# Kernel tuning notes

Measured on AMD Instinct MI355X. Metric: run time of the kernel, lower is better.

The kernel has to match this reference:

```python
import jax, jax.numpy as jnp
import numpy as np
from jax.scipy.special import digamma

# Dims (see init_kwargs): pose P=4 -> D=16, stem A=128, primary caps B=32,
# classes C=10, class-caps kernel K=6 (== primary feature map size), 3 routing iters.
P, D, A, B, C, K, ITER = 4, 16, 128, 32, 10, 6, 3
N = B * K * K                                    # input capsules routed to each class capsule
ALPHA0, KAPPA0, NU0 = 1.0, 1.0, float(D + 1)     # Dirichlet/Normal-Wishart priors (m0=0, Psi0=I, cov='diag')
BN_EPS, EPS = 1e-5, 1e-8


def conv2d(x, w, s):
    return jax.lax.conv_general_dilated(x, w, (s, s), 'VALID',
                                        dimension_numbers=('NCHW', 'OIHW', 'NCHW'))


def bn(x, gamma, beta, axes):
    # batch-norm with batch statistics (training-mode math)
    mu = x.mean(axes, keepdims=True)
    var = x.var(axes, keepdims=True)
    return (x - mu) * jax.lax.rsqrt(var + BN_EPS) * gamma + beta


def setup_inputs():
    key = jax.random.key(0)
    ks = jax.random.split(key, 4)
    f32 = jnp.float32
    x = jax.random.normal(ks[0], (128, 3, 32, 32), dtype=f32)
    conv1_w = jax.random.normal(ks[1], (A, 3, 5, 5), dtype=f32) * 0.1
    bn1_g = jnp.ones((A,), f32); bn1_b = jnp.zeros((A,), f32)
    prim_w = jax.random.normal(ks[2], (B * D + B, A, 3, 3), dtype=f32) * 0.05
    bna_g = jnp.ones((B,), f32); bna_b = jnp.zeros((B,), f32)
    bnp_g = jnp.ones((B,), f32); bnp_b = jnp.zeros((B,), f32)
    W_ij = jax.random.normal(ks[3], (B, C, K, K, P, P), dtype=f32) * 0.3
    return dict(x=x, conv1_w=conv1_w, bn1_g=bn1_g, bn1_b=bn1_b, prim_w=prim_w,
                bna_g=bna_g, bna_b=bna_b, bnp_g=bnp_g, bnp_b=bnp_b, W_ij=W_ij)


def _vb_stats(Ra, V):
    # Ra: (b,N,C) responsibility * input activation; V: (b,N,C,D) votes
    Nj = Ra.sum(1) + EPS                                         # (b,C)
    xbar = jnp.einsum('bnc,bncd->bcd', Ra, V) / Nj[..., None]    # weighted vote mean
    diff = V - xbar[:, None]
    sigma = jnp.einsum('bnc,bncd->bcd', Ra, diff * diff) / Nj[..., None]  # diag cov
    kappa = KAPPA0 + Nj
    m = Nj[..., None] * xbar / kappa[..., None]                  # posterior mean (m0 = 0)
    nu = NU0 + Nj
    Psi = 1.0 + Nj[..., None] * sigma + (KAPPA0 * Nj / kappa)[..., None] * xbar * xbar  # Psi0 = I (diag)
    return Nj, kappa, m, nu, Psi


def _expectations(Nj, nu, Psi, d_idx):
    alpha = ALPHA0 + Nj
    E_lnpi = digamma(alpha) - digamma(alpha.sum(-1, keepdims=True))
    E_lnLam = (digamma(0.5 * (nu[..., None] + 1.0 - d_idx)).sum(-1)
               + D * jnp.log(2.0) - jnp.log(Psi).sum(-1))
    return E_lnpi, E_lnLam


def reference(x, conv1_w, bn1_g, bn1_b, prim_w, bna_g, bna_b, bnp_g, bnp_b, W_ij):
    b = x.shape[0]
    # --- stem: Conv5x5/s2 + BN + ReLU ---
    h = conv2d(x, conv1_w, 2)                                    # (b,A,14,14)
    h = jax.nn.relu(bn(h, bn1_g[None, :, None, None], bn1_b[None, :, None, None], (0, 2, 3)))
    # --- primary capsules: Conv3x3/s2 -> poses + activations ---
    pc = conv2d(h, prim_w, 2)                                    # (b,B*D+B,6,6)
    poses, a = pc[:, :B * D], pc[:, B * D:]
    a = jax.nn.sigmoid(bn(a, bna_g[None, :, None, None], bna_b[None, :, None, None], (0, 2, 3)))
    poses = bn(poses.reshape(b, B, D, K, K),
               bnp_g[None, :, None, None, None], bnp_b[None, :, None, None, None], (0, 2, 3, 4))
    poses = poses.reshape(b, B, P, P, K, K)
    # --- class capsules: votes V = W_ij @ pose, kernel covers whole 6x6 map ---
    V = jnp.einsum('icxypq,biqrxy->bicxypr', W_ij, poses)        # (b,B,C,K,K,P,P)
    V = V.transpose(0, 1, 3, 4, 2, 5, 6).reshape(b, N, C, D)
    a_i = a.reshape(b, N)
    # --- variational Bayes routing (diag Normal-Wishart, ITER iterations) ---
    d_idx = jnp.arange(1, D + 1, dtype=x.dtype)
    R = jnp.full((b, N, C), 1.0 / C, dtype=x.dtype)
    for t in range(ITER):
        Nj, kappa, m, nu, Psi = _vb_stats(R * a_i[:, :, None], V)
        if t < ITER - 1:
            E_lnpi, E_lnLam = _expectations(Nj, nu, Psi, d_idx)
            dm = V - m[:, None]
            quad = D / kappa[:, None, :] + nu[:, None, :] * jnp.einsum('bncd,bcd->bnc', dm * dm, 1.0 / Psi)
            lnp = (E_lnpi[:, None] + 0.5 * E_lnLam[:, None]
                   - 0.5 * D * jnp.log(2.0 * jnp.pi) - 0.5 * quad)
            R = jax.nn.softmax(lnp, axis=-1)
    E_lnpi, E_lnLam = _expectations(Nj, nu, Psi, d_idx)
    logits = E_lnpi + 0.5 * E_lnLam                              # (b,C)
    yhat = jax.nn.sigmoid(bn(logits, 1.0, 0.0, (0,)))            # BatchNorm1d(affine=False)
    return yhat
```

## Files before the change

### kernel.cpp

```cpp
#include <hip/hip_runtime.h>
#include <hip/hip_bf16.h>

#define NB 128
#define AA 128
#define BB 32
#define CC 10
#define KK 6
#define DD 16
#define NN 1152
#define H1 14
#define CH2 544
#define NG 4608
#define KG 1152
#define MG 576

typedef short bfrag8 __attribute__((ext_vector_type(8)));
typedef float facc4 __attribute__((ext_vector_type(4)));

__device__ __forceinline__ unsigned short f2bf(float f) {
    unsigned u = __float_as_uint(f);
    u += 0x7FFF + ((u >> 16) & 1);
    return (unsigned short)(u >> 16);
}
__device__ __forceinline__ float bf2f(unsigned short s) {
    return __uint_as_float(((unsigned)s) << 16);
}

__global__ __launch_bounds__(256, 3) void k_conv1(const float* __restrict__ x,
                                                  const float* __restrict__ w,
                                                  float* __restrict__ h,
                                                  float* __restrict__ part1s,
                                                  float* __restrict__ part1q) {
    __shared__ __align__(16) float sX[3][7][32];
    __shared__ float sWf[AA * 75];
    __shared__ float sS[128], sQ[128];
    const int p = blockIdx.x;
    const int b = blockIdx.y;
    const int tid = threadIdx.x;
    for (int j = tid; j < AA * 75; j += 256) sWf[j] = w[j];
    for (int j = tid; j < 3 * 7 * 32; j += 256) {
        int col = j & 31; int t2 = j >> 5; int row = t2 % 7; int ic = t2 / 7;
        sX[ic][row][col] = x[b * 3072 + ic * 1024 + (4 * p + row) * 32 + col];
    }
    __syncthreads();
    const int oc = tid & 127, ry = tid >> 7;
    const int r = 2 * p + ry;
    float acc[14];
#pragma unroll
    for (int j = 0; j < 14; ++j) acc[j] = 0.f;
    const float* wr = sWf + oc * 75;
#pragma unroll
    for (int ic = 0; ic < 3; ++ic) {
#pragma unroll
        for (int ky = 0; ky < 5; ++ky) {
            const float* xr = &sX[ic][2 * ry + ky][0];
            float row[32];
#pragma unroll
            for (int q = 0; q < 8; ++q) {
                float4 v = *reinterpret_cast<const float4*>(xr + q * 4);
                row[q * 4 + 0] = v.x; row[q * 4 + 1] = v.y;
                row[q * 4 + 2] = v.z; row[q * 4 + 3] = v.w;
            }
            float w0 = wr[ic * 25 + ky * 5 + 0];
            float w1 = wr[ic * 25 + ky * 5 + 1];
            float w2 = wr[ic * 25 + ky * 5 + 2];
            float w3 = wr[ic * 25 + ky * 5 + 3];
            float w4 = wr[ic * 25 + ky * 5 + 4];
#pragma unroll
            for (int ox = 0; ox < 14; ++ox) {
                float s = acc[ox];
                s = fmaf(row[2 * ox + 0], w0, s);
                s = fmaf(row[2 * ox + 1], w1, s);
                s = fmaf(row[2 * ox + 2], w2, s);
                s = fmaf(row[2 * ox + 3], w3, s);
                s = fmaf(row[2 * ox + 4], w4, s);
                acc[ox] = s;
            }
        }
    }
    float* out = h + ((size_t)(b * AA + oc) * 14 + r) * 14;
#pragma unroll
    for (int q = 0; q < 7; ++q)
        *reinterpret_cast<float2*>(out + q * 2) = make_float2(acc[q * 2], acc[q * 2 + 1]);
    float s_th = 0.f, q_th = 0.f;
#pragma unroll
    for (int ox = 0; ox < 14; ++ox) { s_th += acc[ox]; q_th = fmaf(acc[ox], acc[ox], q_th); }
    if (ry == 1) { sS[oc] = s_th; sQ[oc] = q_th; }
    __syncthreads();
    if (ry == 0) {
        int blk = p * 128 + b;
        part1s[oc * 896 + blk] = s_th + sS[oc];
        part1q[oc * 896 + blk] = q_th + sQ[oc];
    }
}

__device__ __forceinline__ void blk_reduce2(float& s, float& s2, int tid) {
#pragma unroll
    for (int o = 32; o > 0; o >>= 1) { s += __shfl_down(s, o); s2 += __shfl_down(s2, o); }
    __shared__ float ls[4], lq[4];
    int lane = tid & 63, wid = tid >> 6;
    if (lane == 0) { ls[wid] = s; lq[wid] = s2; }
    __syncthreads();
    if (tid == 0) {
        s = ls[0] + ls[1] + ls[2] + ls[3];
        s2 = lq[0] + lq[1] + lq[2] + lq[3];
    }
}

__global__ void k_bnred1(const float* __restrict__ part1s, const float* __restrict__ part1q,
                         const float* __restrict__ g, const float* __restrict__ be,
                         float* __restrict__ bn1) {
    int c = blockIdx.x;
    int tid = threadIdx.x;
    float s = 0.f, s2 = 0.f;
    for (int j = tid; j < 896; j += 256) { s += part1s[c * 896 + j]; s2 += part1q[c * 896 + j]; }
    blk_reduce2(s, s2, tid);
    if (tid == 0) {
        const float n = (float)(NB * 196);
        float mu = s / n;
        float var = s2 / n - mu * mu;
        float sc = g[c] * rsqrtf(var + 1e-5f);
        bn1[c] = sc;
        bn1[AA + c] = be[c] - mu * sc;
    }
}

__global__ void k_pim(const float* __restrict__ w, const float* __restrict__ h,
                      const float* __restrict__ bn1,
                      unsigned short* __restrict__ Ah, unsigned short* __restrict__ Al,
                      unsigned short* __restrict__ Bh, unsigned short* __restrict__ Bl) {
    const int blk = blockIdx.x;
    const int tid = threadIdx.x;
    if (blk < 324) {
        int t = blk * 256 + tid;
        int row = t / (KG / 8), seg = t % (KG / 8);
        alignas(16) unsigned short hi[8], lo[8];
        if (row < CH2) {
            const float* src = w + (size_t)row * KG + seg * 8;
#pragma unroll
            for (int j = 0; j < 8; ++j) {
                float v = src[j];
                unsigned short hh = f2bf(v);
                hi[j] = hh;
                lo[j] = f2bf(v - bf2f(hh));
            }
        } else {
#pragma unroll
            for (int j = 0; j < 8; ++j) { hi[j] = 0; lo[j] = 0; }
        }
        *reinterpret_cast<uint4*>(Ah + (size_t)row * KG + seg * 8) = *reinterpret_cast<const uint4*>(hi);
        *reinterpret_cast<uint4*>(Al + (size_t)row * KG + seg * 8) = *reinterpret_cast<const uint4*>(lo);
        return;
    }
    __shared__ float sBn1[2 * AA];
    sBn1[tid] = bn1[tid];
    __syncthreads();
    int t = (blk - 324) * 256 + tid;
    int n = t / (KG / 8), seg = t % (KG / 8);
    int b = n / 36, xy = n % 36;
    int oy = xy / 6, ox = xy % 6;
    const float* hb = h + (size_t)b * (AA * 196) + (2 * oy) * 14 + 2 * ox;
    alignas(16) unsigned short hi[8], lo[8];
#pragma unroll
    for (int j = 0; j < 8; ++j) {
        int k = seg * 8 + j;
        int ic = k / 9, kk = k - ic * 9;
        int ky = kk / 3, kx = kk - ky * 3;
        float v = hb[ic * 196 + ky * 14 + kx];
        v = fmaxf(fmaf(v, sBn1[ic], sBn1[AA + ic]), 0.f);
        unsigned short hh = f2bf(v);
        hi[j] = hh;
        lo[j] = f2bf(v - bf2f(hh));
    }
    *reinterpret_cast<uint4*>(Bh + (size_t)n * KG + seg * 8) = *reinterpret_cast<const uint4*>(hi);
    *reinterpret_cast<uint4*>(Bl + (size_t)n * KG + seg * 8) = *reinterpret_cast<const uint4*>(lo);
}

__global__ __launch_bounds__(256, 4) void k_gemm(const unsigned short* __restrict__ Ah,
                                                 const unsigned short* __restrict__ Al,
                                                 const unsigned short* __restrict__ Bh,
                                                 const unsigned short* __restrict__ Bl,
                                                 float* __restrict__ pcT,
                                                 float* __restrict__ part2) {
    __shared__ alignas(16) unsigned short sAh[64][44], sAl[64][44];
    __shared__ alignas(16) unsigned short sBh[64][44], sBl[64][44];
    __shared__ float sRed[128];
    const int s = blockIdx.x;
    const int k8 = s & 7, j = s >> 3;
    const int jm = j / 9;
    const int y = k8 + 8 * jm;
    const int xg = j - 9 * jm;
    const int oc0 = xg * 64;
    const int n0 = y * 64;
    const int tid = threadIdx.x;
    const int lane = tid & 63, wv = tid >> 6;
    const int wm = wv >> 1, wn = wv & 1;
    const int quad = lane >> 4, r16 = lane & 15;
    const int srow = tid >> 2, sseg = tid & 3;

    facc4 acc[2][2] = {};
    const size_t gA = (size_t)(oc0 + srow) * KG + sseg * 8;
    const size_t gB = (size_t)(n0 + srow) * KG + sseg * 8;

    uint4 vAh = *reinterpret_cast<const uint4*>(Ah + gA);
    uint4 vAl = *reinterpret_cast<const uint4*>(Al + gA);
    uint4 vBh = *reinterpret_cast<const uint4*>(Bh + gB);
    uint4 vBl = *reinterpret_cast<const uint4*>(Bl + gB);

    for (int ks = 0; ks < KG / 32; ++ks) {
        __syncthreads();
        *reinterpret_cast<uint4*>(&sAh[srow][sseg * 8]) = vAh;
        *reinterpret_cast<uint4*>(&sAl[srow][sseg * 8]) = vAl;
        *reinterpret_cast<uint4*>(&sBh[srow][sseg * 8]) = vBh;
        *reinterpret_cast<uint4*>(&sBl[srow][sseg * 8]) = vBl;
        __syncthreads();
        if (ks + 1 < KG / 32) {
            const int k0n = (ks + 1) * 32;
            vAh = *reinterpret_cast<const uint4*>(Ah + gA + k0n);
            vAl = *reinterpret_cast<const uint4*>(Al + gA + k0n);
            vBh = *reinterpret_cast<const uint4*>(Bh + gB + k0n);
            vBl = *reinterpret_cast<const uint4*>(Bl + gB + k0n);
        }
        bfrag8 ah[2], al[2], bh[2], bl[2];
#pragma unroll
        for (int i = 0; i < 2; ++i) {
            ah[i] = *reinterpret_cast<const bfrag8*>(&sAh[wm * 32 + i * 16 + r16][quad * 8]);
            al[i] = *reinterpret_cast<const bfrag8*>(&sAl[wm * 32 + i * 16 + r16][quad * 8]);
            bh[i] = *reinterpret_cast<const bfrag8*>(&sBh[wn * 32 + i * 16 + r16][quad * 8]);
            bl[i] = *reinterpret_cast<const bfrag8*>(&sBl[wn * 32 + i * 16 + r16][quad * 8]);
        }
#pragma unroll
        for (int i = 0; i < 2; ++i)
#pragma unroll
            for (int jj = 0; jj < 2; ++jj) {
                acc[i][jj] = __builtin_amdgcn_mfma_f32_16x16x32_bf16(ah[i], bh[jj], acc[i][jj], 0, 0, 0);
                acc[i][jj] = __builtin_amdgcn_mfma_f32_16x16x32_bf16(ah[i], bl[jj], acc[i][jj], 0, 0, 0);
                acc[i][jj] = __builtin_amdgcn_mfma_f32_16x16x32_bf16(al[i], bh[jj], acc[i][jj], 0, 0, 0);
            }
    }
#pragma unroll
    for (int i = 0; i < 2; ++i) {
        int oc_base = oc0 + wm * 32 + i * 16 + quad * 4;
        if (oc_base >= CH2) continue;
#pragma unroll
        for (int jj = 0; jj < 2; ++jj) {
            int n = n0 + wn * 32 + jj * 16 + r16;
            *reinterpret_cast<facc4*>(pcT + (size_t)n * CH2 + oc_base) = acc[i][jj];
        }
    }
    if (xg < 8) {
        float ps[2], pq[2];
#pragma unroll
        for (int i = 0; i < 2; ++i) {
            float sv = 0.f, qv = 0.f;
#pragma unroll
            for (int jj = 0; jj < 2; ++jj)
#pragma unroll
                for (int comp = 0; comp < 4; ++comp) {
                    float v = acc[i][jj][comp];
                    sv += v; qv = fmaf(v, v, qv);
                }
#pragma unroll
            for (int o = 32; o > 0; o >>= 1) { sv += __shfl_down(sv, o); qv += __shfl_down(qv, o); }
            ps[i] = sv; pq[i] = qv;
        }
        if (lane == 0) {
#pragma unroll
            for (int i = 0; i < 2; ++i) { sRed[wv * 4 + i * 2 + 0] = ps[i]; sRed[wv * 4 + i * 2 + 1] = pq[i]; }
        }
        __syncthreads();
        if (tid < 8) {
            int wm_ = tid >> 2, i_ = (tid >> 1) & 1, sel = tid & 1;
            float v = sRed[(2 * wm_) * 4 + i_ * 2 + sel] + sRed[(2 * wm_ + 1) * 4 + i_ * 2 + sel];
            int g = xg * 4 + wm_ * 2 + i_;
            part2[sel * 2304 + g * 72 + y] = v;
        }
    } else {
        if (wm == 0) {
#pragma unroll
            for (int i = 0; i < 2; ++i)
#pragma unroll
                for (int comp = 0; comp < 4; ++comp) {
                    float v0 = acc[i][0][comp], v1 = acc[i][1][comp];
                    float sv = v0 + v1;
                    float qv = fmaf(v0, v0, v1 * v1);
#pragma unroll
                    for (int o = 8; o > 0; o >>= 1) {
                        sv += __shfl_down(sv, o, 16);
                        qv += __shfl_down(qv, o, 16);
                    }
                    if (r16 == 0) {
                        int idx = ((wv * 4 + quad) * 2 + i) * 4 + comp;
                        sRed[idx] = sv;
                        sRed[64 + idx] = qv;
                    }
                }
        }
        __syncthreads();
        if (tid < 64) {
            int ch = tid >> 1, sel = tid & 1;
            int i_ = ch >> 4, rem = ch & 15, quad_ = rem >> 2, comp_ = rem & 3;
            int base = sel * 64;
            float v = sRed[base + ((0 * 4 + quad_) * 2 + i_) * 4 + comp_] +
                      sRed[base + ((1 * 4 + quad_) * 2 + i_) * 4 + comp_];
            part2[4608 + sel * 2304 + ch * 72 + y] = v;
        }
    }
}

__device__ __forceinline__ float digammaf_(float x) {
    float r = 0.f;
    while (x < 6.f) { r -= 1.f / x; x += 1.f; }
    float xi = 1.f / x;
    float xi2 = xi * xi;
    return r + logf(x) - 0.5f * xi -
           xi2 * (0.0833333333f - xi2 * (0.0083333333f - xi2 * 0.0039682540f));
}

template <int FIRST>
__global__ __launch_bounds__(640) void k_routed(
    const float* __restrict__ pcT, const float* __restrict__ part2,
    const float* __restrict__ bna_g, const float* __restrict__ bna_b,
    const float* __restrict__ bnp_g, const float* __restrict__ bnp_b,
    const float* __restrict__ Wij,
    const float* __restrict__ S0i, const float* __restrict__ S1i, const float* __restrict__ S2i,
    float* __restrict__ S0o, float* __restrict__ S1o, float* __restrict__ S2o) {
    const int b = blockIdx.x >> 1, half = blockIdx.x & 1;
    const int tid = threadIdx.x;
    const int c = tid >> 6, lane = tid & 63;
    __shared__ float sLnp[CC][66];
    __shared__ float sBn2[128];
    __shared__ __align__(16) float sP[64][20];
    __shared__ float sA[64];
    __shared__ float sM[CC][16], sGq[CC][16], sBase[CC];
    if (tid < 64) {
        if (tid < 32) {
            int i = tid;
            float s = 0.f, s2 = 0.f;
            for (int yy = 0; yy < 72; ++yy) { s += part2[i * 72 + yy]; s2 += part2[2304 + i * 72 + yy]; }
            const float n = (float)(NB * DD * 36);
            float mu = s / n, var = s2 / n - mu * mu;
            float sc = bnp_g[i] * rsqrtf(var + 1e-5f);
            sBn2[i] = sc; sBn2[32 + i] = bnp_b[i] - mu * sc;
        } else {
            int ch = tid - 32;
            float s = 0.f, s2 = 0.f;
            for (int yy = 0; yy < 72; ++yy) { s += part2[4608 + ch * 72 + yy]; s2 += part2[6912 + ch * 72 + yy]; }
            const float n = (float)(NB * 36);
            float mu = s / n, var = s2 / n - mu * mu;
            float sc = bna_g[ch] * rsqrtf(var + 1e-5f);
            sBn2[64 + ch] = sc; sBn2[96 + ch] = bna_b[ch] - mu * sc;
        }
    }
    if (!FIRST && tid < 160) {
        int cc = tid >> 4, d = tid & 15;
        int bc = b * CC + cc;
        float njraw = S0i[bc] + S0i[NB * CC + bc];
        float nj = njraw + 1e-8f;
        float kappa = 1.f + nj;
        float nu = 17.f + nj;
        float s1 = S1i[bc * 16 + d] + S1i[(NB * CC + bc) * 16 + d];
        float s2v = S2i[bc * 16 + d] + S2i[(NB * CC + bc) * 16 + d];
        float xbar = s1 / nj;
        float sig = (s2v - 2.f * xbar * s1 + xbar * xbar * njraw) / nj;
        float Psi = 1.f + nj * sig + (nj / kappa) * xbar * xbar;
        sM[cc][d] = nj * xbar / kappa;
        sGq[cc][d] = 0.5f * nu / Psi;
        float term = digammaf_(0.5f * (nu + 1.f - (float)(d + 1))) - logf(Psi);
#pragma unroll
        for (int o = 8; o > 0; o >>= 1) term += __shfl_down(term, o, 16);
        if (d == 0) {
            float asum = 0.f;
#pragma unroll
            for (int k = 0; k < CC; ++k)
                asum += 1.f + S0i[b * CC + k] + S0i[NB * CC + b * CC + k] + 1e-8f;
            float elnlam = 16.f * 0.69314718056f + term;
            float elnpi = digammaf_(1.f + nj) - digammaf_(asum);
            float lb = elnpi + 0.5f * elnlam;
            sBase[cc] = lb - 8.f * 1.83787706641f - 8.f / kappa;
        }
    }
    __syncthreads();
    float mc[16], Gc[16], basec = 0.f;
    if (!FIRST) {
#pragma unroll
        for (int d = 0; d < 16; ++d) { mc[d] = sM[c][d]; Gc[d] = sGq[c][d]; }
        basec = sBase[c];
    }
    float s0 = 0.f, s1[16], s2[16];
#pragma unroll
    for (int d = 0; d < 16; ++d) { s1[d] = 0.f; s2[d] = 0.f; }

#pragma unroll 1
    for (int it = 0; it < 9; ++it) {
        if (tid < 256) {
            int r = tid >> 2, q = tid & 3;
            int n = half * 576 + it * 64 + r;
            int i = n / 36, xy = n - i * 36;
            int row = b * 36 + xy;
            float4 v = *reinterpret_cast<const float4*>(pcT + (size_t)row * CH2 + i * 16 + q * 4);
            float psc = sBn2[i], psh = sBn2[32 + i];
            v.x = fmaf(v.x, psc, psh); v.y = fmaf(v.y, psc, psh);
            v.z = fmaf(v.z, psc, psh); v.w = fmaf(v.w, psc, psh);
            *reinterpret_cast<float4*>(&sP[r][q * 4]) = v;
        } else if (tid < 320) {
            int r = tid - 256;
            int n = half * 576 + it * 64 + r;
            int i = n / 36, xy = n - i * 36;
            int row = b * 36 + xy;
            float va = fmaf(pcT[(size_t)row * CH2 + BB * DD + i], sBn2[64 + i], sBn2[96 + i]);
            sA[r] = 1.f / (1.f + expf(-va));
        }
        __syncthreads();
        const int n = half * 576 + it * 64 + lane;
        const int i = n / 36, xy = n - i * 36;
        const float4* wp = reinterpret_cast<const float4*>(Wij + (((size_t)i * CC + c) * 36 + xy) * 16);
        alignas(16) float P[16], W[16];
        *reinterpret_cast<float4*>(&P[0])  = *reinterpret_cast<const float4*>(&sP[lane][0]);
        *reinterpret_cast<float4*>(&P[4])  = *reinterpret_cast<const float4*>(&sP[lane][4]);
        *reinterpret_cast<float4*>(&P[8])  = *reinterpret_cast<const float4*>(&sP[lane][8]);
        *reinterpret_cast<float4*>(&P[12]) = *reinterpret_cast<const float4*>(&sP[lane][12]);
        *reinterpret_cast<float4*>(&W[0])  = wp[0];
        *reinterpret_cast<float4*>(&W[4])  = wp[1];
        *reinterpret_cast<float4*>(&W[8])  = wp[2];
        *reinterpret_cast<float4*>(&W[12]) = wp[3];
        float V[16];
#pragma unroll
        for (int p = 0; p < 4; ++p)
#pragma unroll
            for (int r = 0; r < 4; ++r)
                V[p * 4 + r] = W[p * 4 + 0] * P[0 + r] + W[p * 4 + 1] * P[4 + r] +
                               W[p * 4 + 2] * P[8 + r] + W[p * 4 + 3] * P[12 + r];
        float av = sA[lane];
        float wgt;
        if (FIRST) {
            wgt = 0.1f * av;
            __syncthreads();
        } else {
            float q = 0.f;
#pragma unroll
            for (int d = 0; d < 16; ++d) {
                float dm = V[d] - mc[d];
                q = fmaf(dm * dm, Gc[d], q);
            }
            float lnp = basec - q;
            sLnp[c][lane] = lnp;
            __syncthreads();
            float mx = -1e30f;
#pragma unroll
            for (int cc = 0; cc < CC; ++cc) mx = fmaxf(mx, sLnp[cc][lane]);
            float ssum = 0.f;
#pragma unroll
            for (int cc = 0; cc < CC; ++cc) ssum += expf(sLnp[cc][lane] - mx);
            wgt = expf(lnp - mx) / ssum * av;
        }
        s0 += wgt;
#pragma unroll
        for (int d = 0; d < 16; ++d) {
            float wv = wgt * V[d];
            s1[d] += wv;
            s2[d] = fmaf(wv, V[d], s2[d]);
        }
    }
#pragma unroll
    for (int o = 32; o > 0; o >>= 1) {
        s0 += __shfl_down(s0, o);
#pragma unroll
        for (int k = 0; k < 16; ++k) {
            s1[k] += __shfl_down(s1[k], o);
            s2[k] += __shfl_down(s2[k], o);
        }
    }
    if (lane == 0) {
        int idx = half * (NB * CC) + b * CC + c;
        S0o[idx] = s0;
#pragma unroll
        for (int k = 0; k < 16; ++k) { S1o[idx * 16 + k] = s1[k]; S2o[idx * 16 + k] = s2[k]; }
    }
}

__global__ void k_final2(const float* __restrict__ S0p, const float* __restrict__ S1p,
                         const float* __restrict__ S2p, float* __restrict__ out) {
    int c = blockIdx.x;
    int b = threadIdx.x;
    int bc = b * CC + c;
    float njraw = S0p[bc] + S0p[NB * CC + bc];
    float nj = njraw + 1e-8f;
    float asum = 0.f;
#pragma unroll
    for (int k = 0; k < CC; ++k)
        asum += 1.f + S0p[b * CC + k] + S0p[NB * CC + b * CC + k] + 1e-8f;
    float kappa = 1.f + nj;
    float nu = 17.f + nj;
    float elnlam = 16.f * 0.69314718056f;
    for (int d = 0; d < 16; ++d) {
        float s1 = S1p[bc * 16 + d] + S1p[(NB * CC + bc) * 16 + d];
        float s2v = S2p[bc * 16 + d] + S2p[(NB * CC + bc) * 16 + d];
        float xbar = s1 / nj;
        float sig = (s2v - 2.f * xbar * s1 + xbar * xbar * njraw) / nj;
        float Psi = 1.f + nj * sig + (nj / kappa) * xbar * xbar;
        elnlam += digammaf_(0.5f * (nu + 1.f - (float)(d + 1))) - logf(Psi);
    }
    float elnpi = digammaf_(1.f + nj) - digammaf_(asum);
    float v = elnpi + 0.5f * elnlam;
    float s = v, s2 = v * v;
#pragma unroll
    for (int o = 32; o > 0; o >>= 1) { s += __shfl_down(s, o); s2 += __shfl_down(s2, o); }
    __shared__ float ls[2], lq[2];
    int lane = b & 63, wid = b >> 6;
    if (lane == 0) { ls[wid] = s; lq[wid] = s2; }
    __syncthreads();
    float mu = (ls[0] + ls[1]) * (1.f / 128.f);
    float var = (lq[0] + lq[1]) * (1.f / 128.f) - mu * mu;
    out[b * CC + c] = 1.f / (1.f + expf(-(v - mu) * rsqrtf(var + 1e-5f)));
}

extern "C" void kernel_launch(void* const* d_in, const int* in_sizes, int n_in,
                              void* d_out, int out_size, void* d_ws, size_t ws_size,
                              hipStream_t stream) {
    (void)in_sizes; (void)n_in; (void)out_size; (void)ws_size;
    const float* x       = (const float*)d_in[0];
    const float* conv1_w = (const float*)d_in[1];
    const float* bn1_g   = (const float*)d_in[2];
    const float* bn1_b   = (const float*)d_in[3];
    const float* prim_w  = (const float*)d_in[4];
    const float* bna_g   = (const float*)d_in[5];
    const float* bna_b   = (const float*)d_in[6];
    const float* bnp_g   = (const float*)d_in[7];
    const float* bnp_b   = (const float*)d_in[8];
    const float* Wij     = (const float*)d_in[9];

    float* ws = (float*)d_ws;
    float* h   = ws;
    float* pcT = ws + 3211264;
    unsigned short* Bh = (unsigned short*)(ws + 5718016);
    unsigned short* Bl = (unsigned short*)(ws + 8372224);
    unsigned short* Ahp = (unsigned short*)(ws + 11026432);
    unsigned short* Alp = (unsigned short*)(ws + 11358208);
    float* bn1    = ws + 11689984;
    float* S0a    = ws + 11690368;
    float* S1a    = ws + 11692928;
    float* S2a    = ws + 11733888;
    float* S0b    = ws + 11774848;
    float* S1b    = ws + 11777408;
    float* S2b    = ws + 11818368;
    float* part1s = ws + 11859328;
    float* part1q = ws + 11974016;
    float* part2  = ws + 12088704;
    float* out    = (float*)d_out;

    k_conv1<<<dim3(7, 128), 256, 0, stream>>>(x, conv1_w, h, part1s, part1q);
    k_bnred1<<<128, 256, 0, stream>>>(part1s, part1q, bn1_g, bn1_b, bn1);
    k_pim<<<2916, 256, 0, stream>>>(prim_w, h, bn1, Ahp, Alp, Bh, Bl);
    k_gemm<<<648, 256, 0, stream>>>(Ahp, Alp, Bh, Bl, pcT, part2);

    k_routed<1><<<256, 640, 0, stream>>>(pcT, part2, bna_g, bna_b, bnp_g, bnp_b, Wij,
                                         S0a, S1a, S2a, S0a, S1a, S2a);
    k_routed<0><<<256, 640, 0, stream>>>(pcT, part2, bna_g, bna_b, bnp_g, bnp_b, Wij,
                                         S0a, S1a, S2a, S0b, S1b, S2b);
    k_routed<0><<<256, 640, 0, stream>>>(pcT, part2, bna_g, bna_b, bnp_g, bnp_b, Wij,
                                         S0b, S1b, S2b, S0a, S1a, S2a);
    k_final2<<<10, 128, 0, stream>>>(S0a, S1a, S2a, out);
}
```

Before: 186.4 us.

## Split routing over six capsule segments and retile conv1 by output-channel groups

The routing kernels now split each batch item's 1152 input capsules across six blocks instead of two. This gives 768 blocks rather than 256 for better GPU occupancy, and each consumer sums six partial statistics instead of two. Conv1 is restructured so each block loads the whole input image and computes 16 output channels across all 14 rows, with block-level partial BN statistics. This shrinks the BN reduction input. In exchange, more partial-sum reads are needed, and 32 of the 256 conv1 threads sit idle.

```diff
diff --git a/kernel.cpp b/kernel.cpp
--- a/kernel.cpp
+++ b/kernel.cpp
@@ -13,6 +13,7 @@
 #define NG 4608
 #define KG 1152
 #define MG 576
+#define NSEG 6
 
 typedef short bfrag8 __attribute__((ext_vector_type(8)));
 typedef float facc4 __attribute__((ext_vector_type(4)));
@@ -26,71 +27,78 @@
     return __uint_as_float(((unsigned)s) << 16);
 }
 
-__global__ __launch_bounds__(256, 3) void k_conv1(const float* __restrict__ x,
-                                                  const float* __restrict__ w,
-                                                  float* __restrict__ h,
-                                                  float* __restrict__ part1s,
-                                                  float* __restrict__ part1q) {
-    __shared__ __align__(16) float sX[3][7][32];
-    __shared__ float sWf[AA * 75];
-    __shared__ float sS[128], sQ[128];
-    const int p = blockIdx.x;
+__global__ __launch_bounds__(256) void k_conv1(const float* __restrict__ x,
+                                               const float* __restrict__ w,
+                                               float* __restrict__ h,
+                                               float* __restrict__ part1s,
+                                               float* __restrict__ part1q) {
+    __shared__ __align__(16) float sX[3][32][36];
+    __shared__ float sW[16][76];
+    __shared__ float sS[224], sQ[224];
+    const int ocg = blockIdx.x;
     const int b = blockIdx.y;
+    const int oc0 = ocg * 16;
     const int tid = threadIdx.x;
-    for (int j = tid; j < AA * 75; j += 256) sWf[j] = w[j];
-    for (int j = tid; j < 3 * 7 * 32; j += 256) {
-        int col = j & 31; int t2 = j >> 5; int row = t2 % 7; int ic = t2 / 7;
-        sX[ic][row][col] = x[b * 3072 + ic * 1024 + (4 * p + row) * 32 + col];
+    for (int j = tid; j < 3072; j += 256) {
+        int ic = j >> 10, rem = j & 1023;
+        sX[ic][rem >> 5][rem & 31] = x[b * 3072 + j];
+    }
+    for (int j = tid; j < 16 * 75; j += 256) {
+        sW[j / 75][j % 75] = w[oc0 * 75 + j];
     }
     __syncthreads();
-    const int oc = tid & 127, ry = tid >> 7;
-    const int r = 2 * p + ry;
+    const bool act = tid < 224;
+    const int oc_l = tid / 14, oy = tid % 14;
     float acc[14];
 #pragma unroll
     for (int j = 0; j < 14; ++j) acc[j] = 0.f;
-    const float* wr = sWf + oc * 75;
-#pragma unroll
-    for (int ic = 0; ic < 3; ++ic) {
-#pragma unroll
-        for (int ky = 0; ky < 5; ++ky) {
-            const float* xr = &sX[ic][2 * ry + ky][0];
-            float row[32];
-#pragma unroll
-            for (int q = 0; q < 8; ++q) {
-                float4 v = *reinterpret_cast<const float4*>(xr + q * 4);
-                row[q * 4 + 0] = v.x; row[q * 4 + 1] = v.y;
-                row[q * 4 + 2] = v.z; row[q * 4 + 3] = v.w;
+    if (act) {
+        const float* wr = &sW[oc_l][0];
+#pragma unroll
+        for (int ic = 0; ic < 3; ++ic) {
+#pragma unroll
+            for (int ky = 0; ky < 5; ++ky) {
+                const float* xr = &sX[ic][2 * oy + ky][0];
+                float row[32];
+#pragma unroll
+                for (int q = 0; q < 8; ++q) {
+                    float4 v = *reinterpret_cast<const float4*>(xr + q * 4);
+                    row[q * 4 + 0] = v.x; row[q * 4 + 1] = v.y;
+                    row[q * 4 + 2] = v.z; row[q * 4 + 3] = v.w;
+                }
+                float w0 = wr[ic * 25 + ky * 5 + 0];
+                float w1 = wr[ic * 25 + ky * 5 + 1];
+                float w2 = wr[ic * 25 + ky * 5 + 2];
+                float w3 = wr[ic * 25 + ky * 5 + 3];
+                float w4 = wr[ic * 25 + ky * 5 + 4];
+#pragma unroll
+                for (int ox = 0; ox < 14; ++ox) {
+                    float s = acc[ox];
+                    s = fmaf(row[2 * ox + 0], w0, s);
+                    s = fmaf(row[2 * ox + 1], w1, s);
+                    s = fmaf(row[2 * ox + 2], w2, s);
+                    s = fmaf(row[2 * ox + 3], w3, s);
+                    s = fmaf(row[2 * ox + 4], w4, s);
+                    acc[ox] = s;
+                }
             }
-            float w0 = wr[ic * 25 + ky * 5 + 0];
-            float w1 = wr[ic * 25 + ky * 5 + 1];
-            float w2 = wr[ic * 25 + ky * 5 + 2];
-            float w3 = wr[ic * 25 + ky * 5 + 3];
-            float w4 = wr[ic * 25 + ky * 5 + 4];
-#pragma unroll
-            for (int ox = 0; ox < 14; ++ox) {
-                float s = acc[ox];
-                s = fmaf(row[2 * ox + 0], w0, s);
-                s = fmaf(row[2 * ox + 1], w1, s);
-                s = fmaf(row[2 * ox + 2], w2, s);
-                s = fmaf(row[2 * ox + 3], w3, s);
-                s = fmaf(row[2 * ox + 4], w4, s);
-                acc[ox] = s;
-            }
-        }
-    }
-    float* out = h + ((size_t)(b * AA + oc) * 14 + r) * 14;
-#pragma unroll
-    for (int q = 0; q < 7; ++q)
-        *reinterpret_cast<float2*>(out + q * 2) = make_float2(acc[q * 2], acc[q * 2 + 1]);
-    float s_th = 0.f, q_th = 0.f;
-#pragma unroll
-    for (int ox = 0; ox < 14; ++ox) { s_th += acc[ox]; q_th = fmaf(acc[ox], acc[ox], q_th); }
-    if (ry == 1) { sS[oc] = s_th; sQ[oc] = q_th; }
+        }
+        float* out = h + ((size_t)(b * AA + oc0 + oc_l) * 14 + oy) * 14;
+#pragma unroll
+        for (int q = 0; q < 7; ++q)
+            *reinterpret_cast<float2*>(out + q * 2) = make_float2(acc[q * 2], acc[q * 2 + 1]);
+        float s_th = 0.f, q_th = 0.f;
+#pragma unroll
+        for (int ox = 0; ox < 14; ++ox) { s_th += acc[ox]; q_th = fmaf(acc[ox], acc[ox], q_th); }
+        sS[tid] = s_th; sQ[tid] = q_th;
+    }
     __syncthreads();
-    if (ry == 0) {
-        int blk = p * 128 + b;
-        part1s[oc * 896 + blk] = s_th + sS[oc];
-        part1q[oc * 896 + blk] = q_th + sQ[oc];
+    if (tid < 16) {
+        float s = 0.f, q = 0.f;
+#pragma unroll
+        for (int r = 0; r < 14; ++r) { s += sS[tid * 14 + r]; q += sQ[tid * 14 + r]; }
+        part1s[(oc0 + tid) * NB + b] = s;
+        part1q[(oc0 + tid) * NB + b] = q;
     }
 }
 
@@ -112,8 +120,8 @@
                          float* __restrict__ bn1) {
     int c = blockIdx.x;
     int tid = threadIdx.x;
-    float s = 0.f, s2 = 0.f;
-    for (int j = tid; j < 896; j += 256) { s += part1s[c * 896 + j]; s2 += part1q[c * 896 + j]; }
+    float s = (tid < NB) ? part1s[c * NB + tid] : 0.f;
+    float s2 = (tid < NB) ? part1q[c * NB + tid] : 0.f;
     blk_reduce2(s, s2, tid);
     if (tid == 0) {
         const float n = (float)(NB * 196);
@@ -325,7 +333,7 @@
     const float* __restrict__ Wij,
     const float* __restrict__ S0i, const float* __restrict__ S1i, const float* __restrict__ S2i,
     float* __restrict__ S0o, float* __restrict__ S1o, float* __restrict__ S2o) {
-    const int b = blockIdx.x >> 1, half = blockIdx.x & 1;
+    const int b = blockIdx.x / NSEG, seg = blockIdx.x % NSEG;
     const int tid = threadIdx.x;
     const int c = tid >> 6, lane = tid & 63;
     __shared__ float sLnp[CC][66];
@@ -355,12 +363,18 @@
     if (!FIRST && tid < 160) {
         int cc = tid >> 4, d = tid & 15;
         int bc = b * CC + cc;
-        float njraw = S0i[bc] + S0i[NB * CC + bc];
+        float njraw = 0.f;
+#pragma unroll
+        for (int sg = 0; sg < NSEG; ++sg) njraw += S0i[sg * (NB * CC) + bc];
         float nj = njraw + 1e-8f;
         float kappa = 1.f + nj;
         float nu = 17.f + nj;
-        float s1 = S1i[bc * 16 + d] + S1i[(NB * CC + bc) * 16 + d];
-        float s2v = S2i[bc * 16 + d] + S2i[(NB * CC + bc) * 16 + d];
+        float s1 = 0.f, s2v = 0.f;
+#pragma unroll
+        for (int sg = 0; sg < NSEG; ++sg) {
+            s1 += S1i[sg * (NB * CC * 16) + bc * 16 + d];
+            s2v += S2i[sg * (NB * CC * 16) + bc * 16 + d];
+        }
         float xbar = s1 / nj;
         float sig = (s2v - 2.f * xbar * s1 + xbar * xbar * njraw) / nj;
         float Psi = 1.f + nj * sig + (nj / kappa) * xbar * xbar;
@@ -372,8 +386,12 @@
         if (d == 0) {
             float asum = 0.f;
 #pragma unroll
-            for (int k = 0; k < CC; ++k)
-                asum += 1.f + S0i[b * CC + k] + S0i[NB * CC + b * CC + k] + 1e-8f;
+            for (int k = 0; k < CC; ++k) {
+                float t = 0.f;
+#pragma unroll
+                for (int sg = 0; sg < NSEG; ++sg) t += S0i[sg * (NB * CC) + b * CC + k];
+                asum += 1.f + t + 1e-8f;
+            }
             float elnlam = 16.f * 0.69314718056f + term;
             float elnpi = digammaf_(1.f + nj) - digammaf_(asum);
             float lb = elnpi + 0.5f * elnlam;
@@ -392,10 +410,10 @@
     for (int d = 0; d < 16; ++d) { s1[d] = 0.f; s2[d] = 0.f; }
 
 #pragma unroll 1
-    for (int it = 0; it < 9; ++it) {
+    for (int it = 0; it < 3; ++it) {
         if (tid < 256) {
             int r = tid >> 2, q = tid & 3;
-            int n = half * 576 + it * 64 + r;
+            int n = seg * 192 + it * 64 + r;
             int i = n / 36, xy = n - i * 36;
             int row = b * 36 + xy;
             float4 v = *reinterpret_cast<const float4*>(pcT + (size_t)row * CH2 + i * 16 + q * 4);
@@ -405,14 +423,14 @@
             *reinterpret_cast<float4*>(&sP[r][q * 4]) = v;
         } else if (tid < 320) {
             int r = tid - 256;
-            int n = half * 576 + it * 64 + r;
+            int n = seg * 192 + it * 64 + r;
             int i = n / 36, xy = n - i * 36;
             int row = b * 36 + xy;
             float va = fmaf(pcT[(size_t)row * CH2 + BB * DD + i], sBn2[64 + i], sBn2[96 + i]);
             sA[r] = 1.f / (1.f + expf(-va));
         }
         __syncthreads();
-        const int n = half * 576 + it * 64 + lane;
+        const int n = seg * 192 + it * 64 + lane;
         const int i = n / 36, xy = n - i * 36;
         const float4* wp = reinterpret_cast<const float4*>(Wij + (((size_t)i * CC + c) * 36 + xy) * 16);
         alignas(16) float P[16], W[16];
@@ -472,7 +490,7 @@
         }
     }
     if (lane == 0) {
-        int idx = half * (NB * CC) + b * CC + c;
+        int idx = seg * (NB * CC) + b * CC + c;
         S0o[idx] = s0;
 #pragma unroll
         for (int k = 0; k < 16; ++k) { S1o[idx * 16 + k] = s1[k]; S2o[idx * 16 + k] = s2[k]; }
@@ -484,18 +502,28 @@
     int c = blockIdx.x;
     int b = threadIdx.x;
     int bc = b * CC + c;
-    float njraw = S0p[bc] + S0p[NB * CC + bc];
+    float njraw = 0.f;
+#pragma unroll
+    for (int sg = 0; sg < NSEG; ++sg) njraw += S0p[sg * (NB * CC) + bc];
     float nj = njraw + 1e-8f;
     float asum = 0.f;
 #pragma unroll
-    for (int k = 0; k < CC; ++k)
-        asum += 1.f + S0p[b * CC + k] + S0p[NB * CC + b * CC + k] + 1e-8f;
+    for (int k = 0; k < CC; ++k) {
+        float t = 0.f;
+#pragma unroll
+        for (int sg = 0; sg < NSEG; ++sg) t += S0p[sg * (NB * CC) + b * CC + k];
+        asum += 1.f + t + 1e-8f;
+    }
     float kappa = 1.f + nj;
     float nu = 17.f + nj;
     float elnlam = 16.f * 0.69314718056f;
     for (int d = 0; d < 16; ++d) {
-        float s1 = S1p[bc * 16 + d] + S1p[(NB * CC + bc) * 16 + d];
-        float s2v = S2p[bc * 16 + d] + S2p[(NB * CC + bc) * 16 + d];
+        float s1 = 0.f, s2v = 0.f;
+#pragma unroll
+        for (int sg = 0; sg < NSEG; ++sg) {
+            s1 += S1p[sg * (NB * CC * 16) + bc * 16 + d];
+            s2v += S2p[sg * (NB * CC * 16) + bc * 16 + d];
+        }
         float xbar = s1 / nj;
         float sig = (s2v - 2.f * xbar * s1 + xbar * xbar * njraw) / nj;
         float Psi = 1.f + nj * sig + (nj / kappa) * xbar * xbar;
@@ -539,26 +567,26 @@
     unsigned short* Alp = (unsigned short*)(ws + 11358208);
     float* bn1    = ws + 11689984;
     float* S0a    = ws + 11690368;
-    float* S1a    = ws + 11692928;
-    float* S2a    = ws + 11733888;
-    float* S0b    = ws + 11774848;
-    float* S1b    = ws + 11777408;
-    float* S2b    = ws + 11818368;
-    float* part1s = ws + 11859328;
-    float* part1q = ws + 11974016;
-    float* part2  = ws + 12088704;
+    float* S1a    = ws + 11698048;
+    float* S2a    = ws + 11820928;
+    float* S0b    = ws + 11943808;
+    float* S1b    = ws + 11951488;
+    float* S2b    = ws + 12074368;
+    float* part1s = ws + 12197248;
+    float* part1q = ws + 12213632;
+    float* part2  = ws + 12230016;
     float* out    = (float*)d_out;
 
-    k_conv1<<<dim3(7, 128), 256, 0, stream>>>(x, conv1_w, h, part1s, part1q);
+    k_conv1<<<dim3(8, 128), 256, 0, stream>>>(x, conv1_w, h, part1s, part1q);
     k_bnred1<<<128, 256, 0, stream>>>(part1s, part1q, bn1_g, bn1_b, bn1);
     k_pim<<<2916, 256, 0, stream>>>(prim_w, h, bn1, Ahp, Alp, Bh, Bl);
     k_gemm<<<648, 256, 0, stream>>>(Ahp, Alp, Bh, Bl, pcT, part2);
 
-    k_routed<1><<<256, 640, 0, stream>>>(pcT, part2, bna_g, bna_b, bnp_g, bnp_b, Wij,
-                                         S0a, S1a, S2a, S0a, S1a, S2a);
-    k_routed<0><<<256, 640, 0, stream>>>(pcT, part2, bna_g, bna_b, bnp_g, bnp_b, Wij,
-                                         S0a, S1a, S2a, S0b, S1b, S2b);
-    k_routed<0><<<256, 640, 0, stream>>>(pcT, part2, bna_g, bna_b, bnp_g, bnp_b, Wij,
-                                         S0b, S1b, S2b, S0a, S1a, S2a);
+    k_routed<1><<<NB * NSEG, 640, 0, stream>>>(pcT, part2, bna_g, bna_b, bnp_g, bnp_b, Wij,
+                                               S0a, S1a, S2a, S0a, S1a, S2a);
+    k_routed<0><<<NB * NSEG, 640, 0, stream>>>(pcT, part2, bna_g, bna_b, bnp_g, bnp_b, Wij,
+                                               S0a, S1a, S2a, S0b, S1b, S2b);
+    k_routed<0><<<NB * NSEG, 640, 0, stream>>>(pcT, part2, bna_g, bna_b, bnp_g, bnp_b, Wij,
+                                               S0b, S1b, S2b, S0a, S1a, S2a);
     k_final2<<<10, 128, 0, stream>>>(S0a, S1a, S2a, out);
 }
```

New measurement: 261.7 us. 40.4% more time.
